# Kernel optimization log

Measured on AMD Instinct MI355X. Metric: run time of the kernel, lower is better.

The kernel has to match this reference:

```python
import jax, jax.numpy as jnp
import numpy as np

N = 100000          # batch_size == number of tree nodes
F = 512             # feature_size
C = 512             # number_of_features_to_detect
WINDOW_DEPTH = 3    # depth_of_sliding_window


def _build_tree(rng, n):
    # random tree: parent[i] < i, node 0 is root (parent[0] = 0)
    parent = np.zeros(n, dtype=np.int32)
    parent[1:] = (rng.random(n - 1) * np.arange(1, n)).astype(np.int32)
    level = np.zeros(n, dtype=np.int32)       # treelib level (root = 0)
    pos = np.zeros(n, dtype=np.int32)         # 0-based index among parent's children
    child_count = np.zeros(n, dtype=np.int32)
    for i in range(1, n):
        p = parent[i]
        level[i] = level[p] + 1
        pos[i] = child_count[p]
        child_count[p] += 1
    sib = child_count[parent] - 1              # treelib siblings() excludes self
    sib[0] = 0                                 # root has no siblings
    pos[0] = 1                                 # special case in get_node_position_amongst_siblings
    return parent, level, pos, sib


def setup_inputs() -> dict:
    key = jax.random.key(0)
    k1, k2, k3, k4, k5 = jax.random.split(key, 5)
    rng = np.random.default_rng(0)
    parent, level, pos, sib = _build_tree(rng, N)
    return {
        "tree_data": jax.random.normal(k1, (N, F), dtype=jnp.float32),
        "W_top": jax.random.normal(k2, (C, F), dtype=jnp.float32),
        "W_left": jax.random.normal(k3, (C, F), dtype=jnp.float32),
        "W_right": jax.random.normal(k4, (C, F), dtype=jnp.float32),
        "bias": jax.random.normal(k5, (C,), dtype=jnp.float32),
        "parent": jnp.asarray(parent),
        "level": jnp.asarray(level),
        "pos": jnp.asarray(pos),
        "sib": jnp.asarray(sib),
    }


def reference(tree_data, W_top, W_left, W_right, bias, parent, level, pos, sib):
    n = tree_data.shape[0]
    f32 = jnp.float32
    # per-node projections with each of the 3 weights: [N, C]
    Yt = tree_data @ W_top.T
    Yl = tree_data @ W_left.T
    Yr = tree_data @ W_right.T
    # edge list: self-edge (window root hovers itself) + child edges
    node_ids = jnp.arange(n, dtype=jnp.int32)
    nodes = jnp.concatenate([node_ids, node_ids[1:]])        # hovered node n_id
    seg = jnp.concatenate([node_ids, parent[1:]])            # window root (output row)
    # coefficients: twc uses the WINDOW ROOT's depth (level+1), rwc/lwc the hovered node
    twc = level[seg].astype(f32) / f32(WINDOW_DEPTH - 1)
    rwc = (1.0 - twc) * ((pos[nodes] - 1).astype(f32)
                         / jnp.maximum(1, sib[nodes] - 1).astype(f32))
    lwc = (1.0 - twc) * (1.0 - rwc)
    contrib = (twc[:, None] * Yt[nodes]
               + lwc[:, None] * Yl[nodes]
               + rwc[:, None] * Yr[nodes]
               + bias)                                        # bias added per hovered node
    summed = jax.ops.segment_sum(contrib, seg, num_segments=n)
    return jnp.tanh(summed)
```

## Files before the change

kernel.cpp:

```cpp
#include <hip/hip_runtime.h>
#include <hip/hip_bf16.h>
#include <stdint.h>

#define F_DIM 512
#define C_DIM 512
#define K3    1536
#define NT    24

typedef _Float16 f16x8 __attribute__((ext_vector_type(8)));
typedef float    f32x4 __attribute__((ext_vector_type(4)));

__device__ __forceinline__ float rho_of(int p, int sb) {
    int d = sb - 1; if (d < 1) d = 1;
    return (float)(p - 1) / (float)d;
}

__device__ __forceinline__ void split2s(float v, _Float16& h, _Float16& m) {
    h = (_Float16)v;
    float r1 = v - (float)h;
    m = (_Float16)(r1 * 2048.0f);
}

__global__ void k_count(const int* __restrict__ parent, int* __restrict__ counts, int n) {
    int c = blockIdx.x * 256 + threadIdx.x;
    if (c >= 1 && c < n) atomicAdd(&counts[parent[c]], 1);
}

__device__ __forceinline__ int blockScanIncl(int v, int* sm) {
    int lane = threadIdx.x & 63;
    int w = threadIdx.x >> 6;
    #pragma unroll
    for (int d = 1; d < 64; d <<= 1) {
        int t = __shfl_up(v, d, 64);
        if (lane >= d) v += t;
    }
    if (lane == 63) sm[w] = v;
    __syncthreads();
    if (threadIdx.x < 64) {
        int s = (threadIdx.x < 16) ? sm[threadIdx.x] : 0;
        #pragma unroll
        for (int d = 1; d < 16; d <<= 1) {
            int t = __shfl_up(s, d, 64);
            if (lane >= d) s += t;
        }
        if (threadIdx.x < 16) sm[threadIdx.x] = s;
    }
    __syncthreads();
    return v + (w > 0 ? sm[w - 1] : 0);
}

__global__ void k_scan1(const int* __restrict__ counts, int* __restrict__ starts,
                        int* __restrict__ bsums, int n) {
    __shared__ int sm[16];
    int i = blockIdx.x * 1024 + threadIdx.x;
    int v = (i < n) ? counts[i] : 0;
    int incl = blockScanIncl(v, sm);
    if (i < n) starts[i] = incl - v;
    if (threadIdx.x == 1023) bsums[blockIdx.x] = incl;
}

__global__ void k_scan2(int* __restrict__ bsums, int nb) {
    __shared__ int sm[16];
    int v = ((int)threadIdx.x < nb) ? bsums[threadIdx.x] : 0;
    int incl = blockScanIncl(v, sm);
    if ((int)threadIdx.x < nb) bsums[threadIdx.x] = incl - v;
}

__global__ void k_scan3(int* __restrict__ starts, const int* __restrict__ bsums, int n) {
    int i = blockIdx.x * 1024 + threadIdx.x;
    if (i < n) starts[i] += bsums[blockIdx.x];
}

__global__ void k_fill(const int* __restrict__ parent, const int* __restrict__ pos,
                       const int* __restrict__ starts, int* __restrict__ childlist, int n) {
    int c = blockIdx.x * 256 + threadIdx.x;
    if (c >= 1 && c < n) childlist[starts[parent[c]] + pos[c]] = c;
}

__global__ void k_bcat(const float* __restrict__ Wt, const float* __restrict__ Wl,
                       const float* __restrict__ Wr,
                       _Float16* __restrict__ Bh, _Float16* __restrict__ Bm) {
    int i = blockIdx.x * 256 + threadIdx.x;
    if (i >= C_DIM * K3) return;
    int j = i / K3, kk = i - j * K3;
    int sec = kk >> 9, f = kk & 511;
    const float* W = (sec == 0) ? Wt : ((sec == 1) ? Wl : Wr);
    float v = W[j * F_DIM + f];
    _Float16 h, m;
    split2s(v, h, m);
    Bh[i] = h; Bm[i] = m;
}

__global__ __launch_bounds__(256)
void k_agg(const float* __restrict__ x, const int* __restrict__ level,
           const int* __restrict__ pos, const int* __restrict__ sib,
           const int* __restrict__ starts, const int* __restrict__ counts,
           const int* __restrict__ childlist,
           _Float16* __restrict__ Ah, _Float16* __restrict__ Am,
           int node0, int cnt) {
    int lane = threadIdx.x & 63;
    int gw = (blockIdx.x * 256 + threadIdx.x) >> 6;
    int nW = (gridDim.x * 256) >> 6;
    for (int i = gw; i < cnt; i += nW) {
        int s = node0 + i;
        float t = 0.5f * (float)level[s];
        float u = 1.0f - t;
        float u2 = u * u;
        float s0[8], s1[8];
        #pragma unroll
        for (int j = 0; j < 8; ++j) { s0[j] = 0.f; s1[j] = 0.f; }
        {
            float r = rho_of(pos[s], sib[s]);
            const float4* xp = (const float4*)(x + (size_t)s * F_DIM) + lane * 2;
            float4 a = xp[0], b = xp[1];
            float vv[8] = {a.x, a.y, a.z, a.w, b.x, b.y, b.z, b.w};
            #pragma unroll
            for (int j = 0; j < 8; ++j) { s0[j] += vv[j]; s1[j] = fmaf(r, vv[j], s1[j]); }
        }
        int cs = starts[s], ne = counts[s];
        for (int e = 0; e < ne; ++e) {
            int c = childlist[cs + e];
            float r = rho_of(pos[c], sib[c]);
            const float4* xp = (const float4*)(x + (size_t)c * F_DIM) + lane * 2;
            float4 a = xp[0], b = xp[1];
            float vv[8] = {a.x, a.y, a.z, a.w, b.x, b.y, b.z, b.w};
            #pragma unroll
            for (int j = 0; j < 8; ++j) { s0[j] += vv[j]; s1[j] = fmaf(r, vv[j], s1[j]); }
        }
        f16x8 ph[3], pm[3];
        #pragma unroll
        for (int j = 0; j < 8; ++j) {
            float a0 = t * s0[j];
            float a1 = fmaf(-u2, s1[j], u * s0[j]);
            float a2 = u * s1[j];
            _Float16 h, m;
            split2s(a0, h, m); ph[0][j] = h; pm[0][j] = m;
            split2s(a1, h, m); ph[1][j] = h; pm[1][j] = m;
            split2s(a2, h, m); ph[2][j] = h; pm[2][j] = m;
        }
        size_t rb = (size_t)i * K3 + (size_t)(lane * 8);
        #pragma unroll
        for (int sec = 0; sec < 3; ++sec) {
            *(f16x8*)(Ah + rb + sec * 512) = ph[sec];
            *(f16x8*)(Am + rb + sec * 512) = pm[sec];
        }
    }
}

__device__ __forceinline__ void stageTile(const char* gbase, _Float16* lds) {
    int tid = threadIdx.x;
    int wid = tid >> 6;
    #pragma unroll
    for (int rnd = 0; rnd < 4; ++rnd) {
        int c = rnd * 256 + tid;
        int row = c >> 3;
        int gslot = (c & 7) ^ (row & 7);
        const void* gp = gbase + (size_t)row * (K3 * 2) + ((size_t)gslot << 4);
        _Float16* lp = lds + (size_t)(rnd * 256 + wid * 64) * 8;
        __builtin_amdgcn_global_load_lds(
            (const __attribute__((address_space(1))) unsigned int*)gp,
            (__attribute__((address_space(3))) unsigned int*)lp, 16, 0, 0);
    }
}

__device__ __forceinline__ f32x4 mfma16(f16x8 a, f16x8 b, f32x4 c) {
    return __builtin_amdgcn_mfma_f32_16x16x32_f16(a, b, c, 0, 0, 0);
}

__device__ __forceinline__ void compute_step(
    const _Float16* cAh, const _Float16* cAm, const _Float16* cBh, const _Float16* cBm,
    int wm, int wn, int l15, int koff0, int koff1,
    f32x4 (&accH)[4][4], f32x4 (&accR)[4][4])
{
    #pragma unroll
    for (int kc = 0; kc < 2; ++kc) {
        int ko = kc ? koff1 : koff0;
        f16x8 ah[4], am[4], bh[4], bm[4];
        #pragma unroll
        for (int ni = 0; ni < 4; ++ni) {
            int co = (wn * 64 + ni * 16 + l15) * 64;
            bh[ni] = *(const f16x8*)&cBh[co + ko];
            bm[ni] = *(const f16x8*)&cBm[co + ko];
        }
        #pragma unroll
        for (int mi = 0; mi < 4; ++mi) {
            int ro = (wm * 64 + mi * 16 + l15) * 64;
            ah[mi] = *(const f16x8*)&cAh[ro + ko];
            am[mi] = *(const f16x8*)&cAm[ro + ko];
        }
        #pragma unroll
        for (int mi = 0; mi < 4; ++mi) {
            #pragma unroll
            for (int ni = 0; ni < 4; ++ni) {
                accH[mi][ni] = mfma16(ah[mi], bh[ni], accH[mi][ni]);
                accR[mi][ni] = mfma16(ah[mi], bm[ni], accR[mi][ni]);
                accR[mi][ni] = mfma16(am[mi], bh[ni], accR[mi][ni]);
            }
        }
    }
}

__global__ __launch_bounds__(256, 2)
void k_gemm(const _Float16* __restrict__ Ah, const _Float16* __restrict__ Am,
            const _Float16* __restrict__ Bh, const _Float16* __restrict__ Bm,
            const float* __restrict__ bias, const int* __restrict__ counts,
            float* __restrict__ out, int Mreal, int row0) {
    __shared__ __align__(16) _Float16 sAh[128 * 64];
    __shared__ __align__(16) _Float16 sAm[128 * 64];
    __shared__ __align__(16) _Float16 sBh[128 * 64];
    __shared__ __align__(16) _Float16 sBm[128 * 64];

    int nwg = gridDim.x, bid = blockIdx.x;
    int q = nwg >> 3, r = nwg & 7;
    int xcd = bid & 7, idx = bid >> 3;
    int wg = (xcd < r ? xcd * (q + 1) : r * (q + 1) + (xcd - r) * q) + idx;
    int panel = wg >> 2, colt = wg & 3;
    int m0 = panel * 128, n0 = colt * 128;

    int lane = threadIdx.x & 63, wid = threadIdx.x >> 6;
    int wm = wid >> 1, wn = wid & 1;
    int l15 = lane & 15, lg = lane >> 4, lx = lane & 7;

    const char* gAh = (const char*)(Ah + (size_t)m0 * K3);
    const char* gAm = (const char*)(Am + (size_t)m0 * K3);
    const char* gBh = (const char*)(Bh + (size_t)n0 * K3);
    const char* gBm = (const char*)(Bm + (size_t)n0 * K3);

    f32x4 accH[4][4] = {};
    f32x4 accR[4][4] = {};

    int koff0 = ((((0 << 2) + lg) ^ lx) << 3);
    int koff1 = ((((1 << 2) + lg) ^ lx) << 3);

    for (int t = 0; t < NT; ++t) {
        size_t kb = (size_t)t * 128;
        stageTile(gAh + kb, sAh); stageTile(gAm + kb, sAm);
        stageTile(gBh + kb, sBh); stageTile(gBm + kb, sBm);
        __syncthreads();

        compute_step(sAh, sAm, sBh, sBm, wm, wn, l15, koff0, koff1, accH, accR);

        __syncthreads();
    }

    const float S1 = 1.0f / 2048.0f;

    #pragma unroll
    for (int mi = 0; mi < 4; ++mi) {
        #pragma unroll
        for (int ni = 0; ni < 4; ++ni) {
            int colL = n0 + wn * 64 + ni * 16 + l15;
            #pragma unroll
            for (int rr = 0; rr < 4; ++rr) {
                int rowL = m0 + wm * 64 + mi * 16 + lg * 4 + rr;
                if (rowL < Mreal) {
                    int g = row0 + rowL;
                    float v = accH[mi][ni][rr]
                              + accR[mi][ni][rr] * S1
                              + (1.0f + (float)counts[g]) * bias[colL];
                    out[(size_t)g * C_DIM + colL] = tanhf(v);
                }
            }
        }
    }
}

extern "C" void kernel_launch(void* const* d_in, const int* in_sizes, int n_in,
                              void* d_out, int out_size, void* d_ws, size_t ws_size,
                              hipStream_t stream) {
    const float* x    = (const float*)d_in[0];
    const float* Wt   = (const float*)d_in[1];
    const float* Wl   = (const float*)d_in[2];
    const float* Wr   = (const float*)d_in[3];
    const float* bias = (const float*)d_in[4];
    const int* parent = (const int*)d_in[5];
    const int* level  = (const int*)d_in[6];
    const int* pos    = (const int*)d_in[7];
    const int* sib    = (const int*)d_in[8];
    const int N = in_sizes[5];
    float* out = (float*)d_out;
    (void)n_in; (void)out_size;

    char* w = (char*)d_ws;
    size_t off = 0;
    auto alloc = [&](size_t bytes) -> void* {
        void* p = w + off;
        off += (bytes + 255) & ~(size_t)255;
        return p;
    };
    int* counts    = (int*)alloc((size_t)N * 4);
    int* starts    = (int*)alloc((size_t)N * 4);
    int* childlist = (int*)alloc((size_t)N * 4);
    int* bsums     = (int*)alloc(1024 * 4);
    _Float16* Bh   = (_Float16*)alloc((size_t)C_DIM * K3 * 2);
    _Float16* Bm   = (_Float16*)alloc((size_t)C_DIM * K3 * 2);

    size_t avail = ws_size > off ? ws_size - off : 0;
    long long Npad = ((long long)N + 127) & ~127LL;
    long long chunkM = (long long)(avail / ((size_t)K3 * 2 * 2)) & ~127LL;
    if (chunkM > Npad) chunkM = Npad;
    if (chunkM < 128) chunkM = 128;
    _Float16* Ah = (_Float16*)alloc((size_t)chunkM * K3 * 2);
    _Float16* Am = (_Float16*)alloc((size_t)chunkM * K3 * 2);

    hipMemsetAsync(counts, 0, (size_t)N * 4, stream);
    int nb256 = (N + 255) / 256;
    int nb1024 = (N + 1023) / 1024;
    k_count<<<nb256, 256, 0, stream>>>(parent, counts, N);
    k_scan1<<<nb1024, 1024, 0, stream>>>(counts, starts, bsums, N);
    k_scan2<<<1, 1024, 0, stream>>>(bsums, nb1024);
    k_scan3<<<nb1024, 1024, 0, stream>>>(starts, bsums, N);
    k_fill<<<nb256, 256, 0, stream>>>(parent, pos, starts, childlist, N);
    k_bcat<<<(C_DIM * K3 + 255) / 256, 256, 0, stream>>>(Wt, Wl, Wr, Bh, Bm);

    for (long long m0 = 0; m0 < N; m0 += chunkM) {
        int mc = (int)((N - m0 < chunkM) ? (N - m0) : chunkM);
        int mcPad = (mc + 127) & ~127;
        k_agg<<<2048, 256, 0, stream>>>(x, level, pos, sib, starts, counts, childlist,
                                        Ah, Am, (int)m0, mc);
        int ntiles = (mcPad / 128) * 4;
        k_gemm<<<ntiles, 256, 0, stream>>>(Ah, Am, Bh, Bm, bias, counts,
                                           out, mc, (int)m0);
    }
}
```

Baseline: 768.0 us.

## Double-buffer GEMM LDS tiles with K=32 steps to overlap loads and MFMA

Splits the K loop into 48 steps of 32 instead of 24 steps of 64, and stages the next tile into a second LDS buffer while computing on the current one. A partial vmcnt wait lets the next tile's loads stay in flight. Fragments are loaded into registers before a barrier so the next prefetch cannot overwrite them, and the MFMA block runs at raised wave priority. This hides global-to-LDS latency behind compute, but doubles the number of barriers and shrinks the work per step. The LDS swizzle is also changed to match the narrower tile.

```diff
diff --git a/kernel.cpp b/kernel.cpp
--- a/kernel.cpp
+++ b/kernel.cpp
@@ -5,7 +5,7 @@
 #define F_DIM 512
 #define C_DIM 512
 #define K3    1536
-#define NT    24
+#define NT    48
 
 typedef _Float16 f16x8 __attribute__((ext_vector_type(8)));
 typedef float    f32x4 __attribute__((ext_vector_type(4)));
@@ -147,47 +147,108 @@
     }
 }
 
-__device__ __forceinline__ void stageTile(const char* gbase, _Float16* lds) {
-    int tid = threadIdx.x;
-    int wid = tid >> 6;
-    #pragma unroll
-    for (int rnd = 0; rnd < 4; ++rnd) {
-        int c = rnd * 256 + tid;
-        int row = c >> 3;
-        int gslot = (c & 7) ^ (row & 7);
-        const void* gp = gbase + (size_t)row * (K3 * 2) + ((size_t)gslot << 4);
-        _Float16* lp = lds + (size_t)(rnd * 256 + wid * 64) * 8;
-        __builtin_amdgcn_global_load_lds(
-            (const __attribute__((address_space(1))) unsigned int*)gp,
-            (__attribute__((address_space(3))) unsigned int*)lp, 16, 0, 0);
-    }
-}
-
 __device__ __forceinline__ f32x4 mfma16(f16x8 a, f16x8 b, f32x4 c) {
     return __builtin_amdgcn_mfma_f32_16x16x32_f16(a, b, c, 0, 0, 0);
 }
 
-__device__ __forceinline__ void compute_step(
-    const _Float16* cAh, const _Float16* cAm, const _Float16* cBh, const _Float16* cBm,
-    int wm, int wn, int l15, int koff0, int koff1,
-    f32x4 (&accH)[4][4], f32x4 (&accR)[4][4])
-{
-    #pragma unroll
-    for (int kc = 0; kc < 2; ++kc) {
-        int ko = kc ? koff1 : koff0;
+#define AS1 __attribute__((address_space(1)))
+#define AS3 __attribute__((address_space(3)))
+
+__global__ __launch_bounds__(256, 2)
+void k_gemm(const _Float16* __restrict__ Ah, const _Float16* __restrict__ Am,
+            const _Float16* __restrict__ Bh, const _Float16* __restrict__ Bm,
+            const float* __restrict__ bias, const int* __restrict__ counts,
+            float* __restrict__ out, int Mreal, int row0) {
+    __shared__ __align__(16) _Float16 sAh[2][128 * 32];
+    __shared__ __align__(16) _Float16 sAm[2][128 * 32];
+    __shared__ __align__(16) _Float16 sBh[2][128 * 32];
+    __shared__ __align__(16) _Float16 sBm[2][128 * 32];
+
+    int nwg = gridDim.x, bid = blockIdx.x;
+    int q = nwg >> 3, r = nwg & 7;
+    int xcd = bid & 7, idx = bid >> 3;
+    int wg = (xcd < r ? xcd * (q + 1) : r * (q + 1) + (xcd - r) * q) + idx;
+    int panel = wg >> 2, colt = wg & 3;
+    int m0 = panel * 128, n0 = colt * 128;
+
+    int tid = threadIdx.x;
+    int lane = tid & 63, wid = tid >> 6;
+    int wm = wid >> 1, wn = wid & 1;
+    int l15 = lane & 15, lg = lane >> 4;
+
+    int c0 = tid,        r0 = c0 >> 2, s0g = (c0 & 3) ^ ((r0 >> 1) & 3);
+    int c1 = 256 + tid,  r1 = c1 >> 2, s1g = (c1 & 3) ^ ((r1 >> 1) & 3);
+    size_t so0 = (size_t)r0 * (K3 * 2) + (size_t)(s0g << 4);
+    size_t so1 = (size_t)r1 * (K3 * 2) + (size_t)(s1g << 4);
+    const char* gAh0 = (const char*)(Ah + (size_t)m0 * K3) + so0;
+    const char* gAh1 = (const char*)(Ah + (size_t)m0 * K3) + so1;
+    const char* gAm0 = (const char*)(Am + (size_t)m0 * K3) + so0;
+    const char* gAm1 = (const char*)(Am + (size_t)m0 * K3) + so1;
+    const char* gBh0 = (const char*)(Bh + (size_t)n0 * K3) + so0;
+    const char* gBh1 = (const char*)(Bh + (size_t)n0 * K3) + so1;
+    const char* gBm0 = (const char*)(Bm + (size_t)n0 * K3) + so0;
+    const char* gBm1 = (const char*)(Bm + (size_t)n0 * K3) + so1;
+    int ld0 = (0 * 256 + wid * 64) * 8;
+    int ld1 = (1 * 256 + wid * 64) * 8;
+
+    int koff = ((lg ^ ((l15 >> 1) & 3)) << 3);
+
+    f32x4 accH[4][4] = {};
+    f32x4 accR[4][4] = {};
+
+#define STAGE(pb, kb)                                                                      \
+    do {                                                                                   \
+        __builtin_amdgcn_global_load_lds((const AS1 unsigned int*)(gAh0 + (kb)),           \
+            (AS3 unsigned int*)(&sAh[pb][ld0]), 16, 0, 0);                                 \
+        __builtin_amdgcn_global_load_lds((const AS1 unsigned int*)(gAh1 + (kb)),           \
+            (AS3 unsigned int*)(&sAh[pb][ld1]), 16, 0, 0);                                 \
+        __builtin_amdgcn_global_load_lds((const AS1 unsigned int*)(gAm0 + (kb)),           \
+            (AS3 unsigned int*)(&sAm[pb][ld0]), 16, 0, 0);                                 \
+        __builtin_amdgcn_global_load_lds((const AS1 unsigned int*)(gAm1 + (kb)),           \
+            (AS3 unsigned int*)(&sAm[pb][ld1]), 16, 0, 0);                                 \
+        __builtin_amdgcn_global_load_lds((const AS1 unsigned int*)(gBh0 + (kb)),           \
+            (AS3 unsigned int*)(&sBh[pb][ld0]), 16, 0, 0);                                 \
+        __builtin_amdgcn_global_load_lds((const AS1 unsigned int*)(gBh1 + (kb)),           \
+            (AS3 unsigned int*)(&sBh[pb][ld1]), 16, 0, 0);                                 \
+        __builtin_amdgcn_global_load_lds((const AS1 unsigned int*)(gBm0 + (kb)),           \
+            (AS3 unsigned int*)(&sBm[pb][ld0]), 16, 0, 0);                                 \
+        __builtin_amdgcn_global_load_lds((const AS1 unsigned int*)(gBm1 + (kb)),           \
+            (AS3 unsigned int*)(&sBm[pb][ld1]), 16, 0, 0);                                 \
+    } while (0)
+
+    STAGE(0, 0);
+
+    for (int t = 0; t < NT; ++t) {
+        int p = t & 1;
+        if (t + 1 < NT) {
+            STAGE(p ^ 1, (size_t)(t + 1) * 64);
+            asm volatile("s_waitcnt vmcnt(8)" ::: "memory");
+        } else {
+            asm volatile("s_waitcnt vmcnt(0)" ::: "memory");
+        }
+        __builtin_amdgcn_sched_barrier(0);
+        __builtin_amdgcn_s_barrier();
+        __builtin_amdgcn_sched_barrier(0);
+
         f16x8 ah[4], am[4], bh[4], bm[4];
         #pragma unroll
         for (int ni = 0; ni < 4; ++ni) {
-            int co = (wn * 64 + ni * 16 + l15) * 64;
-            bh[ni] = *(const f16x8*)&cBh[co + ko];
-            bm[ni] = *(const f16x8*)&cBm[co + ko];
+            int co = (wn * 64 + ni * 16 + l15) * 32 + koff;
+            bh[ni] = *(const f16x8*)&sBh[p][co];
+            bm[ni] = *(const f16x8*)&sBm[p][co];
         }
         #pragma unroll
         for (int mi = 0; mi < 4; ++mi) {
-            int ro = (wm * 64 + mi * 16 + l15) * 64;
-            ah[mi] = *(const f16x8*)&cAh[ro + ko];
-            am[mi] = *(const f16x8*)&cAm[ro + ko];
-        }
+            int ro = (wm * 64 + mi * 16 + l15) * 32 + koff;
+            ah[mi] = *(const f16x8*)&sAh[p][ro];
+            am[mi] = *(const f16x8*)&sAm[p][ro];
+        }
+        asm volatile("s_waitcnt lgkmcnt(0)" ::: "memory");
+        __builtin_amdgcn_sched_barrier(0);
+        __builtin_amdgcn_s_barrier();
+        __builtin_amdgcn_sched_barrier(0);
+
+        __builtin_amdgcn_s_setprio(1);
         #pragma unroll
         for (int mi = 0; mi < 4; ++mi) {
             #pragma unroll
@@ -197,51 +258,10 @@
                 accR[mi][ni] = mfma16(am[mi], bh[ni], accR[mi][ni]);
             }
         }
-    }
-}
-
-__global__ __launch_bounds__(256, 2)
-void k_gemm(const _Float16* __restrict__ Ah, const _Float16* __restrict__ Am,
-            const _Float16* __restrict__ Bh, const _Float16* __restrict__ Bm,
-            const float* __restrict__ bias, const int* __restrict__ counts,
-            float* __restrict__ out, int Mreal, int row0) {
-    __shared__ __align__(16) _Float16 sAh[128 * 64];
-    __shared__ __align__(16) _Float16 sAm[128 * 64];
-    __shared__ __align__(16) _Float16 sBh[128 * 64];
-    __shared__ __align__(16) _Float16 sBm[128 * 64];
-
-    int nwg = gridDim.x, bid = blockIdx.x;
-    int q = nwg >> 3, r = nwg & 7;
-    int xcd = bid & 7, idx = bid >> 3;
-    int wg = (xcd < r ? xcd * (q + 1) : r * (q + 1) + (xcd - r) * q) + idx;
-    int panel = wg >> 2, colt = wg & 3;
-    int m0 = panel * 128, n0 = colt * 128;
-
-    int lane = threadIdx.x & 63, wid = threadIdx.x >> 6;
-    int wm = wid >> 1, wn = wid & 1;
-    int l15 = lane & 15, lg = lane >> 4, lx = lane & 7;
-
-    const char* gAh = (const char*)(Ah + (size_t)m0 * K3);
-    const char* gAm = (const char*)(Am + (size_t)m0 * K3);
-    const char* gBh = (const char*)(Bh + (size_t)n0 * K3);
-    const char* gBm = (const char*)(Bm + (size_t)n0 * K3);
-
-    f32x4 accH[4][4] = {};
-    f32x4 accR[4][4] = {};
-
-    int koff0 = ((((0 << 2) + lg) ^ lx) << 3);
-    int koff1 = ((((1 << 2) + lg) ^ lx) << 3);
-
-    for (int t = 0; t < NT; ++t) {
-        size_t kb = (size_t)t * 128;
-        stageTile(gAh + kb, sAh); stageTile(gAm + kb, sAm);
-        stageTile(gBh + kb, sBh); stageTile(gBm + kb, sBm);
-        __syncthreads();
-
-        compute_step(sAh, sAm, sBh, sBm, wm, wn, l15, koff0, koff1, accH, accR);
-
-        __syncthreads();
-    }
+        __builtin_amdgcn_s_setprio(0);
+        __builtin_amdgcn_sched_barrier(0);
+    }
+#undef STAGE
 
     const float S1 = 1.0f / 2048.0f;
 
```

New measurement: 824.9 us. 1.07x slower.
